# Kernel tuning notes

Hardware: AMD Instinct MI355X
Metric: run time of the kernel (lower is better)

## Reference

```python
import jax, jax.numpy as jnp
import numpy as np

N = 4194304
C = 10

def setup_inputs() -> dict:
    key = jax.random.key(0)
    k1, k2 = jax.random.split(key)
    predicted = jax.random.normal(k1, (N, C), dtype=jnp.float32)
    target = jax.random.uniform(k2, (N, C), dtype=jnp.float32)
    return {"predicted": predicted, "target": target}

def reference(predicted, target):
    # Equivalent to: for y in range(C): cum += target[:, y] * cross_entropy(pred, y)
    # i.e. mean over points of -sum_y target[:, y] * log_softmax(pred)[:, y]
    logp = jax.nn.log_softmax(predicted, axis=-1)  # [N, C]
    cum_losses = -jnp.sum(target * logp, axis=-1)  # [N]
    return jnp.mean(cum_losses)
```

## Files before the change

### kernel.cpp

```cpp
#include <hip/hip_runtime.h>
#include <hip/hip_bf16.h>


#define N_ROWS 4194304
#define C_DIM 10
#define ROWS_PER_THREAD 2
#define BLOCK 256

__global__ __launch_bounds__(BLOCK) void kl_loss_kernel(
    const float* __restrict__ pred,
    const float* __restrict__ tgt,
    float* __restrict__ out)
{
    const int tid = blockIdx.x * BLOCK + threadIdx.x;

    const float4* p4 = reinterpret_cast<const float4*>(pred) + (size_t)tid * 5;
    const float4* t4 = reinterpret_cast<const float4*>(tgt)  + (size_t)tid * 5;

    float p[20], t[20];
#pragma unroll
    for (int i = 0; i < 5; ++i) {
        float4 a = p4[i];
        p[4 * i + 0] = a.x; p[4 * i + 1] = a.y; p[4 * i + 2] = a.z; p[4 * i + 3] = a.w;
    }
#pragma unroll
    for (int i = 0; i < 5; ++i) {
        float4 a = t4[i];
        t[4 * i + 0] = a.x; t[4 * i + 1] = a.y; t[4 * i + 2] = a.z; t[4 * i + 3] = a.w;
    }

    float local = 0.0f;
#pragma unroll
    for (int r = 0; r < ROWS_PER_THREAD; ++r) {
        const float* x  = p + r * C_DIM;
        const float* ty = t + r * C_DIM;

        float m = x[0];
#pragma unroll
        for (int i = 1; i < C_DIM; ++i) m = fmaxf(m, x[i]);

        float s = 0.0f, dot = 0.0f, st = 0.0f;
#pragma unroll
        for (int i = 0; i < C_DIM; ++i) {
            s   += __expf(x[i] - m);
            dot  = fmaf(ty[i], x[i], dot);
            st  += ty[i];
        }
        float lse = m + __logf(s);
        local += st * lse - dot;
    }

#pragma unroll
    for (int off = 32; off > 0; off >>= 1)
        local += __shfl_down(local, off, 64);

    __shared__ float sdata[BLOCK / 64];
    const int lane = threadIdx.x & 63;
    const int wid  = threadIdx.x >> 6;
    if (lane == 0) sdata[wid] = local;
    __syncthreads();

    if (threadIdx.x == 0) {
        float b = sdata[0] + sdata[1] + sdata[2] + sdata[3];
        atomicAdd(out, b * (1.0f / (float)N_ROWS));
    }
}

extern "C" void kernel_launch(void* const* d_in, const int* in_sizes, int n_in,
                              void* d_out, int out_size, void* d_ws, size_t ws_size,
                              hipStream_t stream)
{
    const float* pred = (const float*)d_in[0];
    const float* tgt  = (const float*)d_in[1];
    float* out = (float*)d_out;

    hipMemsetAsync(out, 0, sizeof(float), stream);

    const int threads = N_ROWS / ROWS_PER_THREAD;
    const int blocks  = threads / BLOCK;
    kl_loss_kernel<<<blocks, BLOCK, 0, stream>>>(pred, tgt, out);
}
```

Before: 344.8 us.

## Coalesce global loads via block-strided float4 reads and LDS transpose

Each thread now loads float4s strided by block size, so consecutive lanes read consecutive 16-byte words instead of each thread reading a private 80-byte chunk. Predictions are transposed into padded shared memory so each thread can compute a row's log-sum-exp, which goes into a shared per-row array. The loss is then accumulated elementwise from registers. The aim is better memory coalescing on a bandwidth-bound kernel, at the cost of extra LDS traffic, two extra barriers and about 22 KB of LDS per block, which may reduce occupancy.

After: 346.0 us. Within noise of the previous version (+0.4%).

```diff
diff --git a/kernel.cpp b/kernel.cpp
--- a/kernel.cpp
+++ b/kernel.cpp
@@ -4,64 +4,93 @@
 
 #define N_ROWS 4194304
 #define C_DIM 10
-#define ROWS_PER_THREAD 2
 #define BLOCK 256
+#define ROWS_PER_BLOCK 512
+#define WORDS_PER_BLOCK (ROWS_PER_BLOCK * C_DIM)
+#define F4_PER_THREAD 5
+#define LDS_PAD 513
 
 __global__ __launch_bounds__(BLOCK) void kl_loss_kernel(
     const float* __restrict__ pred,
     const float* __restrict__ tgt,
     float* __restrict__ out)
 {
-    const int tid = blockIdx.x * BLOCK + threadIdx.x;
+    __shared__ float sp[C_DIM][LDS_PAD];
+    __shared__ float slse[ROWS_PER_BLOCK];
+    __shared__ float sred[BLOCK / 64];
 
-    const float4* p4 = reinterpret_cast<const float4*>(pred) + (size_t)tid * 5;
-    const float4* t4 = reinterpret_cast<const float4*>(tgt)  + (size_t)tid * 5;
+    const int tid = threadIdx.x;
+    const size_t blk_f4 = (size_t)blockIdx.x * (WORDS_PER_BLOCK / 4);
 
-    float p[20], t[20];
+    const float4* p4 = reinterpret_cast<const float4*>(pred);
+    const float4* t4 = reinterpret_cast<const float4*>(tgt);
+
+    float4 pv[F4_PER_THREAD], tv[F4_PER_THREAD];
 #pragma unroll
-    for (int i = 0; i < 5; ++i) {
-        float4 a = p4[i];
-        p[4 * i + 0] = a.x; p[4 * i + 1] = a.y; p[4 * i + 2] = a.z; p[4 * i + 3] = a.w;
+    for (int i = 0; i < F4_PER_THREAD; ++i)
+        pv[i] = p4[blk_f4 + i * BLOCK + tid];
+#pragma unroll
+    for (int i = 0; i < F4_PER_THREAD; ++i)
+        tv[i] = t4[blk_f4 + i * BLOCK + tid];
+
+#pragma unroll
+    for (int i = 0; i < F4_PER_THREAD; ++i) {
+        int w = (i * BLOCK + tid) * 4;
+        int r = w / C_DIM;
+        int y = w - r * C_DIM;
+        float e[4] = {pv[i].x, pv[i].y, pv[i].z, pv[i].w};
+#pragma unroll
+        for (int c = 0; c < 4; ++c) {
+            sp[y][r] = e[c];
+            ++y;
+            if (y == C_DIM) { y = 0; ++r; }
+        }
     }
+    __syncthreads();
+
 #pragma unroll
-    for (int i = 0; i < 5; ++i) {
-        float4 a = t4[i];
-        t[4 * i + 0] = a.x; t[4 * i + 1] = a.y; t[4 * i + 2] = a.z; t[4 * i + 3] = a.w;
-    }
-
-    float local = 0.0f;
+    for (int half = 0; half < 2; ++half) {
+        int r = tid + half * BLOCK;
+        float x[C_DIM];
 #pragma unroll
-    for (int r = 0; r < ROWS_PER_THREAD; ++r) {
-        const float* x  = p + r * C_DIM;
-        const float* ty = t + r * C_DIM;
-
+        for (int y = 0; y < C_DIM; ++y) x[y] = sp[y][r];
         float m = x[0];
 #pragma unroll
-        for (int i = 1; i < C_DIM; ++i) m = fmaxf(m, x[i]);
+        for (int y = 1; y < C_DIM; ++y) m = fmaxf(m, x[y]);
+        float s = 0.0f;
+#pragma unroll
+        for (int y = 0; y < C_DIM; ++y) s += __expf(x[y] - m);
+        slse[r] = m + __logf(s);
+    }
+    __syncthreads();
 
-        float s = 0.0f, dot = 0.0f, st = 0.0f;
+    float acc = 0.0f;
 #pragma unroll
-        for (int i = 0; i < C_DIM; ++i) {
-            s   += __expf(x[i] - m);
-            dot  = fmaf(ty[i], x[i], dot);
-            st  += ty[i];
+    for (int i = 0; i < F4_PER_THREAD; ++i) {
+        int w = (i * BLOCK + tid) * 4;
+        int r = w / C_DIM;
+        int y = w - r * C_DIM;
+        float pe[4] = {pv[i].x, pv[i].y, pv[i].z, pv[i].w};
+        float te[4] = {tv[i].x, tv[i].y, tv[i].z, tv[i].w};
+#pragma unroll
+        for (int c = 0; c < 4; ++c) {
+            acc = fmaf(te[c], slse[r] - pe[c], acc);
+            ++y;
+            if (y == C_DIM) { y = 0; ++r; }
         }
-        float lse = m + __logf(s);
-        local += st * lse - dot;
     }
 
 #pragma unroll
     for (int off = 32; off > 0; off >>= 1)
-        local += __shfl_down(local, off, 64);
+        acc += __shfl_down(acc, off, 64);
 
-    __shared__ float sdata[BLOCK / 64];
-    const int lane = threadIdx.x & 63;
-    const int wid  = threadIdx.x >> 6;
-    if (lane == 0) sdata[wid] = local;
+    const int lane = tid & 63;
+    const int wid  = tid >> 6;
+    if (lane == 0) sred[wid] = acc;
     __syncthreads();
 
-    if (threadIdx.x == 0) {
-        float b = sdata[0] + sdata[1] + sdata[2] + sdata[3];
+    if (tid == 0) {
+        float b = sred[0] + sred[1] + sred[2] + sred[3];
         atomicAdd(out, b * (1.0f / (float)N_ROWS));
     }
 }
@@ -76,7 +105,6 @@
 
     hipMemsetAsync(out, 0, sizeof(float), stream);
 
-    const int threads = N_ROWS / ROWS_PER_THREAD;
-    const int blocks  = threads / BLOCK;
+    const int blocks = N_ROWS / ROWS_PER_BLOCK;
     kl_loss_kernel<<<blocks, BLOCK, 0, stream>>>(pred, tgt, out);
 }
```
